# Kernel optimization log

Hardware: AMD Instinct MI355X
Metric: run time of the kernel (lower is better)

## Reference

```python
import jax, jax.numpy as jnp
import numpy as np

F = 128
E = 100000   # num_edges
T = 1000000  # num_triplets


def setup_inputs() -> dict:
    key = jax.random.key(0)
    ks = jax.random.split(key, 20)
    s = 0.05
    return {
        "f": jax.random.normal(ks[0], (E, 2 * F), jnp.float32),
        "M01": jax.random.normal(ks[1], (T, F), jnp.float32),
        "M02": jax.random.normal(ks[2], (T, F), jnp.float32),
        # split_net MLP([2F, 2F, 2F]): Linear -> act -> Linear
        "W1": jax.random.normal(ks[3], (2 * F, 2 * F), jnp.float32) * s,
        "b1": jnp.zeros((2 * F,), jnp.float32),
        "W2": jax.random.normal(ks[4], (2 * F, 2 * F), jnp.float32) * s,
        "b2": jnp.zeros((2 * F,), jnp.float32),
        "Ws01": jax.random.normal(ks[5], (F, F), jnp.float32) * s,
        "bs01": jnp.zeros((F,), jnp.float32),
        "Ws02": jax.random.normal(ks[6], (F, F), jnp.float32) * s,
        "bs02": jnp.zeros((F,), jnp.float32),
        "Ws": jax.random.normal(ks[7], (2 * F, F), jnp.float32) * s,
        "bs": jnp.zeros((F,), jnp.float32),
        "Wout": jax.random.normal(ks[8], (F, F), jnp.float32) * s,
        "bout": jnp.zeros((F,), jnp.float32),
        "num_edges": E,
        "idx_ji": jax.random.randint(ks[9], (T,), 0, E, jnp.int32),
        "idx_ki": jax.random.randint(ks[10], (T,), 0, E, jnp.int32),
    }


def reference(f, M01, M02, W1, b1, W2, b2, Ws01, bs01, Ws02, bs02, Ws, bs,
              Wout, bout, num_edges, idx_ji, idx_ki):
    act = jax.nn.silu
    # f = act(split_net(f)); split_net = Linear -> act -> Linear
    h = act(act(f @ W1 + b1) @ W2 + b2)          # [E, 2F]
    f01, f02 = jnp.split(h, 2, axis=-1)           # [E, F] each
    # triplet interaction: gather -> multiply -> linear -> act
    s01 = act((f01[idx_ki] * M01 * f01[idx_ji]) @ Ws01 + bs01)  # [T, F]
    s02 = act((f02[idx_ki] * M02 * f02[idx_ji]) @ Ws02 + bs02)  # [T, F]
    s = act(jnp.concatenate((s01, s02), axis=-1) @ Ws + bs)     # [T, F]
    # scatter-sum triplets back to edges
    out = jax.ops.segment_sum(s, idx_ji, num_segments=num_edges)  # [E, F]
    return out @ Wout + bout
```

## Files before the change

kernel.cpp:

```cpp
#include <hip/hip_runtime.h>

typedef __attribute__((ext_vector_type(8))) short short8;
typedef __attribute__((ext_vector_type(4))) float f32x4;

__device__ __forceinline__ float silu_f(float x) { return x / (1.0f + __expf(-x)); }

__device__ __forceinline__ unsigned short f2bf(float x) {
  unsigned u = __float_as_uint(x);
  u += 0x7FFFu + ((u >> 16) & 1u);
  return (unsigned short)(u >> 16);
}
__device__ __forceinline__ float bf2f(unsigned short v) {
  return __uint_as_float(((unsigned)v) << 16);
}
__device__ __forceinline__ unsigned cvtpk_bf16(float lo, float hi) {
  unsigned r;
  asm("v_cvt_pk_bf16_f32 %0, %1, %2" : "=v"(r) : "v"(lo), "v"(hi));
  return r;
}

#define LGKM_SB() do { asm volatile("s_waitcnt lgkmcnt(0)" ::: "memory"); \
                       __builtin_amdgcn_sched_barrier(0); } while (0)

__device__ __forceinline__ void prep_one(const float* __restrict__ W,
                                         unsigned short* __restrict__ wh,
                                         unsigned short* __restrict__ wl,
                                         int N, int e)
{
  int k = e / N, n = e % N;
  float w = W[e];
  unsigned short hi = f2bf(w);
  unsigned short lo = f2bf(w - bf2f(hi));
  int kp = k >> 6, kk = k & 63;
  size_t dst = (size_t)kp * N * 64 + (size_t)n * 64 + ((((kk >> 3) ^ (n & 7)) << 3)) + (kk & 7);
  wh[dst] = hi;
  wl[dst] = lo;
}

__global__ void prep_all(const float* __restrict__ W1, unsigned short* w1h, unsigned short* w1l,
                         const float* __restrict__ W2, unsigned short* w2h, unsigned short* w2l,
                         const float* __restrict__ Wo, unsigned short* woh, unsigned short* wol)
{
  int e = blockIdx.x * 256 + threadIdx.x;
  if (e < 256 * 256) {
    prep_one(W1, w1h, w1l, 256, e);
    prep_one(W2, w2h, w2l, 256, e);
  }
  if (e < 128 * 128) prep_one(Wo, woh, wol, 128, e);
}

template<int INBF, int ASPLIT>
__global__ __launch_bounds__(512)
void mlp_gemm(const void* A_, const unsigned short* __restrict__ wh,
              const unsigned short* __restrict__ wl,
              const float* __restrict__ bias, unsigned short* __restrict__ C, int M)
{
  __shared__ unsigned short aTh[64 * 64], aTl[64 * 64];
  __shared__ unsigned short whb[256 * 64], wlb[256 * 64];
  const int tid = threadIdx.x;
  const int lane = tid & 63, wv = tid >> 6;
  const int g = wv & 3, hh = wv >> 2;
  const int l15 = lane & 15, l4 = lane >> 4;
  const int row0 = blockIdx.x * 64;
  const int r = tid >> 3, kseg = (tid & 7) * 8;
  const f32x4 zero4 = {0.f, 0.f, 0.f, 0.f};

  f32x4 acc[8];
#pragma unroll
  for (int nt = 0; nt < 8; nt++) acc[nt] = zero4;

  for (int kp = 0; kp < 4; kp++) {
    {
      const int grow = row0 + r;
      float x[8];
      if (grow < M) {
        if (INBF) {
          short8 v = *(const short8*)((const unsigned short*)A_ + (size_t)grow * 256 + kp * 64 + kseg);
#pragma unroll
          for (int j = 0; j < 8; j++) x[j] = bf2f((unsigned short)v[j]);
        } else {
          const float* ap = (const float*)A_ + (size_t)grow * 256 + kp * 64 + kseg;
          float4 v0 = *(const float4*)ap;
          float4 v1 = *(const float4*)(ap + 4);
          x[0] = v0.x; x[1] = v0.y; x[2] = v0.z; x[3] = v0.w;
          x[4] = v1.x; x[5] = v1.y; x[6] = v1.z; x[7] = v1.w;
        }
      } else {
#pragma unroll
        for (int j = 0; j < 8; j++) x[j] = 0.f;
      }
      union { short8 s; unsigned short us[8]; } H, L;
#pragma unroll
      for (int j = 0; j < 8; j++) {
        H.us[j] = f2bf(x[j]);
        L.us[j] = ASPLIT ? f2bf(x[j] - bf2f(H.us[j])) : (unsigned short)0;
      }
      const int dst = r * 64 + ((((kseg >> 3) ^ (r & 7)) << 3));
      *(short8*)(aTh + dst) = H.s;
      if (ASPLIT) *(short8*)(aTl + dst) = L.s;
    }
    {
      const short8* srcH = (const short8*)(wh + (size_t)kp * 16384);
      const short8* srcL = (const short8*)(wl + (size_t)kp * 16384);
#pragma unroll
      for (int i = 0; i < 4; i++) {
        ((short8*)whb)[tid + 512 * i] = srcH[tid + 512 * i];
        ((short8*)wlb)[tid + 512 * i] = srcL[tid + 512 * i];
      }
    }
    __syncthreads();
#pragma unroll
    for (int ks = 0; ks < 2; ks++) {
      const int arow = 16 * g + l15;
      const int aof = arow * 64 + (((4 * ks + l4) ^ (arow & 7)) << 3);
      short8 ah = *(const short8*)(aTh + aof);
      short8 al = *(const short8*)(aTl + aof);
#pragma unroll
      for (int nt = 0; nt < 8; nt++) {
        const int col = 128 * hh + 16 * nt + l15;
        const int bof = col * 64 + (((4 * ks + l4) ^ (col & 7)) << 3);
        short8 bh = *(const short8*)(whb + bof);
        short8 bl = *(const short8*)(wlb + bof);
        acc[nt] = __builtin_amdgcn_mfma_f32_16x16x32_bf16(ah, bh, acc[nt], 0, 0, 0);
        acc[nt] = __builtin_amdgcn_mfma_f32_16x16x32_bf16(ah, bl, acc[nt], 0, 0, 0);
        if (ASPLIT)
          acc[nt] = __builtin_amdgcn_mfma_f32_16x16x32_bf16(al, bh, acc[nt], 0, 0, 0);
      }
    }
    __syncthreads();
  }
#pragma unroll
  for (int nt = 0; nt < 8; nt++) {
    const int col = 128 * hh + 16 * nt + l15;
    const float bv = bias[col];
#pragma unroll
    for (int i = 0; i < 4; i++) {
      const int row = row0 + 16 * g + 4 * l4 + i;
      if (row < M) C[(size_t)row * 256 + col] = f2bf(silu_f(acc[nt][i] + bv));
    }
  }
}

__global__ __launch_bounds__(512)
void final_gemm(const float* __restrict__ A, const unsigned short* __restrict__ wh,
                const unsigned short* __restrict__ wl,
                const float* __restrict__ bias, float* __restrict__ C, int M)
{
  __shared__ unsigned short aTh[64 * 64], aTl[64 * 64];
  __shared__ unsigned short whb[128 * 64], wlb[128 * 64];
  const int tid = threadIdx.x;
  const int lane = tid & 63, wv = tid >> 6;
  const int g = wv & 3, hh = wv >> 2;
  const int l15 = lane & 15, l4 = lane >> 4;
  const int row0 = blockIdx.x * 64;
  const int r = tid >> 3, kseg = (tid & 7) * 8;
  const f32x4 zero4 = {0.f, 0.f, 0.f, 0.f};

  f32x4 acc[4];
#pragma unroll
  for (int nt = 0; nt < 4; nt++) acc[nt] = zero4;

  for (int kp = 0; kp < 2; kp++) {
    {
      const int grow = row0 + r;
      float x[8];
      if (grow < M) {
        const float* ap = A + (size_t)grow * 128 + kp * 64 + kseg;
        float4 v0 = *(const float4*)ap;
        float4 v1 = *(const float4*)(ap + 4);
        x[0] = v0.x; x[1] = v0.y; x[2] = v0.z; x[3] = v0.w;
        x[4] = v1.x; x[5] = v1.y; x[6] = v1.z; x[7] = v1.w;
      } else {
#pragma unroll
        for (int j = 0; j < 8; j++) x[j] = 0.f;
      }
      union { short8 s; unsigned short us[8]; } H, L;
#pragma unroll
      for (int j = 0; j < 8; j++) {
        H.us[j] = f2bf(x[j]);
        L.us[j] = f2bf(x[j] - bf2f(H.us[j]));
      }
      const int dst = r * 64 + ((((kseg >> 3) ^ (r & 7)) << 3));
      *(short8*)(aTh + dst) = H.s;
      *(short8*)(aTl + dst) = L.s;
    }
    {
      const short8* srcH = (const short8*)(wh + (size_t)kp * 8192);
      const short8* srcL = (const short8*)(wl + (size_t)kp * 8192);
#pragma unroll
      for (int i = 0; i < 2; i++) {
        ((short8*)whb)[tid + 512 * i] = srcH[tid + 512 * i];
        ((short8*)wlb)[tid + 512 * i] = srcL[tid + 512 * i];
      }
    }
    __syncthreads();
#pragma unroll
    for (int ks = 0; ks < 2; ks++) {
      const int arow = 16 * g + l15;
      const int aof = arow * 64 + (((4 * ks + l4) ^ (arow & 7)) << 3);
      short8 ah = *(const short8*)(aTh + aof);
      short8 al = *(const short8*)(aTl + aof);
#pragma unroll
      for (int nt = 0; nt < 4; nt++) {
        const int col = 64 * hh + 16 * nt + l15;
        const int bof = col * 64 + (((4 * ks + l4) ^ (col & 7)) << 3);
        short8 bh = *(const short8*)(whb + bof);
        short8 bl = *(const short8*)(wlb + bof);
        acc[nt] = __builtin_amdgcn_mfma_f32_16x16x32_bf16(ah, bh, acc[nt], 0, 0, 0);
        acc[nt] = __builtin_amdgcn_mfma_f32_16x16x32_bf16(ah, bl, acc[nt], 0, 0, 0);
        acc[nt] = __builtin_amdgcn_mfma_f32_16x16x32_bf16(al, bh, acc[nt], 0, 0, 0);
      }
    }
    __syncthreads();
  }
#pragma unroll
  for (int nt = 0; nt < 4; nt++) {
    const int col = 64 * hh + 16 * nt + l15;
    const float bv = bias[col];
#pragma unroll
    for (int i = 0; i < 4; i++) {
      const int row = row0 + 16 * g + 4 * l4 + i;
      if (row < M) C[(size_t)row * 128 + col] = acc[nt][i] + bv;
    }
  }
}

__global__ void hist_k(const int* __restrict__ ji, int* __restrict__ cnt, int T) {
  int t = blockIdx.x * 256 + threadIdx.x;
  const int stride = gridDim.x * 256;
  for (; t < T; t += stride) atomicAdd(&cnt[ji[t]], 1);
}

__global__ void scan1_k(const int* __restrict__ cnt, int* __restrict__ csum, int E) {
  __shared__ int red[256];
  const int c0 = blockIdx.x * 2048;
  int s = 0;
  for (int i = threadIdx.x; i < 2048; i += 256) {
    int e = c0 + i;
    if (e < E) s += cnt[e];
  }
  red[threadIdx.x] = s;
  __syncthreads();
  for (int o = 128; o > 0; o >>= 1) {
    if (threadIdx.x < o) red[threadIdx.x] += red[threadIdx.x + o];
    __syncthreads();
  }
  if (threadIdx.x == 0) csum[blockIdx.x] = red[0];
}

__global__ void scan2_k(int* __restrict__ csum, int n) {
  if (threadIdx.x == 0 && blockIdx.x == 0) {
    int acc = 0;
    for (int i = 0; i < n; i++) { int v = csum[i]; csum[i] = acc; acc += v; }
  }
}

__global__ void scan3_k(const int* __restrict__ cnt, const int* __restrict__ csum,
                        int* __restrict__ off, int E) {
  __shared__ int ts[256];
  const int c0 = blockIdx.x * 2048;
  const int tid = threadIdx.x;
  int loc[8];
  int s = 0;
#pragma unroll
  for (int k = 0; k < 8; k++) {
    int e = c0 + tid * 8 + k;
    loc[k] = (e < E) ? cnt[e] : 0;
    s += loc[k];
  }
  ts[tid] = s;
  __syncthreads();
  for (int o = 1; o < 256; o <<= 1) {
    int v = (tid >= o) ? ts[tid - o] : 0;
    __syncthreads();
    ts[tid] += v;
    __syncthreads();
  }
  int base = csum[blockIdx.x] + ((tid > 0) ? ts[tid - 1] : 0);
#pragma unroll
  for (int k = 0; k < 8; k++) {
    int e = c0 + tid * 8 + k;
    if (e < E) { off[e] = base; base += loc[k]; }
  }
}

__global__ void scatter_k(const int* __restrict__ ji, int* __restrict__ cursor,
                          int* __restrict__ perm, int T) {
  int t = blockIdx.x * 256 + threadIdx.x;
  const int stride = gridDim.x * 256;
  for (; t < T; t += stride) {
    int e = ji[t];
    int p = atomicAdd(&cursor[e], 1);
    perm[p] = t;
  }
}

__device__ __forceinline__ short8 pack8p(const short8 a, const short8 b,
                                         const float4 m0, const float4 m1)
{
  float p0 = bf2f((unsigned short)a[0]) * m0.x * bf2f((unsigned short)b[0]);
  float p1 = bf2f((unsigned short)a[1]) * m0.y * bf2f((unsigned short)b[1]);
  float p2 = bf2f((unsigned short)a[2]) * m0.z * bf2f((unsigned short)b[2]);
  float p3 = bf2f((unsigned short)a[3]) * m0.w * bf2f((unsigned short)b[3]);
  float p4 = bf2f((unsigned short)a[4]) * m1.x * bf2f((unsigned short)b[4]);
  float p5 = bf2f((unsigned short)a[5]) * m1.y * bf2f((unsigned short)b[5]);
  float p6 = bf2f((unsigned short)a[6]) * m1.z * bf2f((unsigned short)b[6]);
  float p7 = bf2f((unsigned short)a[7]) * m1.w * bf2f((unsigned short)b[7]);
  union { short8 s; unsigned u[4]; } t;
  t.u[0] = cvtpk_bf16(p0, p1);
  t.u[1] = cvtpk_bf16(p2, p3);
  t.u[2] = cvtpk_bf16(p4, p5);
  t.u[3] = cvtpk_bf16(p6, p7);
  return t.s;
}

__global__ __launch_bounds__(512, 2)
void triplet_fused(const unsigned short* __restrict__ h,
                   const float* __restrict__ M01, const float* __restrict__ M02,
                   const float* __restrict__ Ws01, const float* __restrict__ bs01,
                   const float* __restrict__ Ws02, const float* __restrict__ bs02,
                   const float* __restrict__ Ws,   const float* __restrict__ bs,
                   const int* __restrict__ idx_ji, const int* __restrict__ idx_ki,
                   const int* __restrict__ perm,
                   float* __restrict__ out_acc, int T)
{
  __shared__ unsigned short wF01[16384];
  __shared__ unsigned short wF02[16384];
  __shared__ unsigned short wFA[16384];
  __shared__ unsigned short wFB[16384];
  __shared__ unsigned short sbuf[8][2048];

  const int tid = threadIdx.x;
  for (int e = tid; e < 16384; e += 512) {
    const int j = e & 7, ln = (e >> 3) & 63, ks = (e >> 9) & 3, ct = e >> 11;
    const int col = 16 * ct + (ln & 15);
    const int k = 32 * ks + 8 * (ln >> 4) + j;
    const int src = k * 128 + col;
    wF01[e] = f2bf(Ws01[src]);
    wF02[e] = f2bf(Ws02[src]);
    wFA[e]  = f2bf(Ws[src]);
    wFB[e]  = f2bf(Ws[16384 + src]);
  }
  __syncthreads();

  const int lane = tid & 63, wv = tid >> 6;
  const int l15 = lane & 15, l4 = lane >> 4;
  unsigned short* const sb = sbuf[wv];
  const f32x4 zero4 = {0.f, 0.f, 0.f, 0.f};

  float bs01v[8], bs02v[8], bsv[8];
#pragma unroll
  for (int ct = 0; ct < 8; ct++) {
    bs01v[ct] = bs01[16 * ct + l15];
    bs02v[ct] = bs02[16 * ct + l15];
    bsv[ct]   = bs[16 * ct + l15];
  }

  const int nsub = T >> 4;
  const int stride = gridDim.x * 8;
  int sub = blockIdx.x * 8 + wv;

  int pidx = perm[(sub << 4) + l15];
  int ek = idx_ki[pidx], ej = idx_ji[pidx];

  for (; sub < nsub; sub += stride) {
    const unsigned short* fa = h + (size_t)ek * 256 + 8 * l4;
    const unsigned short* fb = h + (size_t)ej * 256 + 8 * l4;
    const float* mm1 = M01 + (size_t)pidx * 128 + 8 * l4;
    const float* mm2 = M02 + (size_t)pidx * 128 + 8 * l4;
    short8 ra1[4], rb1[4], ra2[4], rb2[4];
    float4 rm1[8], rm2[8];
#pragma unroll
    for (int ks = 0; ks < 4; ks++) {
      ra1[ks] = *(const short8*)(fa + 32 * ks);
      rb1[ks] = *(const short8*)(fb + 32 * ks);
      rm1[2 * ks]     = *(const float4*)(mm1 + 32 * ks);
      rm1[2 * ks + 1] = *(const float4*)(mm1 + 32 * ks + 4);
      ra2[ks] = *(const short8*)(fa + 128 + 32 * ks);
      rb2[ks] = *(const short8*)(fb + 128 + 32 * ks);
      rm2[2 * ks]     = *(const float4*)(mm2 + 32 * ks);
      rm2[2 * ks + 1] = *(const float4*)(mm2 + 32 * ks + 4);
    }

    const int subn = sub + stride;
    int sidx = (subn << 4) + l15;
    if (sidx >= T) sidx = T - 1;
    const int pidx_n = perm[sidx];

    f32x4 acc1[8];
#pragma unroll
    for (int ct = 0; ct < 8; ct++) acc1[ct] = zero4;
    __builtin_amdgcn_s_setprio(1);
#pragma unroll
    for (int ks = 0; ks < 4; ks++) {
      const short8 a = pack8p(ra1[ks], rb1[ks], rm1[2 * ks], rm1[2 * ks + 1]);
#pragma unroll
      for (int ct = 0; ct < 8; ct++) {
        const short8 b = *(const short8*)(wF01 + ((ct * 4 + ks) * 64 + lane) * 8);
        acc1[ct] = __builtin_amdgcn_mfma_f32_16x16x32_bf16(a, b, acc1[ct], 0, 0, 0);
      }
    }
    __builtin_amdgcn_s_setprio(0);

#pragma unroll
    for (int ct = 0; ct < 8; ct++) {
      const int chi = 2 * ct + (l15 >> 3);
#pragma unroll
      for (int i = 0; i < 4; i++) {
        const int row = 4 * l4 + i;
        sb[row * 128 + (((chi ^ (row & 7)) << 3)) + (l15 & 7)] =
            f2bf(silu_f(acc1[ct][i] + bs01v[ct]));
      }
    }
    LGKM_SB();
    short8 as1[4];
#pragma unroll
    for (int ks = 0; ks < 4; ks++)
      as1[ks] = *(const short8*)(sb + l15 * 128 + (((4 * ks + l4) ^ (l15 & 7)) << 3));

    f32x4 acc3[8];
#pragma unroll
    for (int ct = 0; ct < 8; ct++) acc3[ct] = zero4;
    __builtin_amdgcn_s_setprio(1);
#pragma unroll
    for (int ks = 0; ks < 4; ks++)
#pragma unroll
      for (int ct = 0; ct < 8; ct++) {
        const short8 b = *(const short8*)(wFA + ((ct * 4 + ks) * 64 + lane) * 8);
        acc3[ct] = __builtin_amdgcn_mfma_f32_16x16x32_bf16(as1[ks], b, acc3[ct], 0, 0, 0);
      }
    __builtin_amdgcn_s_setprio(0);

    const int ekn = idx_ki[pidx_n], ejn = idx_ji[pidx_n];

#pragma unroll
    for (int ct = 0; ct < 8; ct++) acc1[ct] = zero4;
    __builtin_amdgcn_s_setprio(1);
#pragma unroll
    for (int ks = 0; ks < 4; ks++) {
      const short8 a = pack8p(ra2[ks], rb2[ks], rm2[2 * ks], rm2[2 * ks + 1]);
#pragma unroll
      for (int ct = 0; ct < 8; ct++) {
        const short8 b = *(const short8*)(wF02 + ((ct * 4 + ks) * 64 + lane) * 8);
        acc1[ct] = __builtin_amdgcn_mfma_f32_16x16x32_bf16(a, b, acc1[ct], 0, 0, 0);
      }
    }
    __builtin_amdgcn_s_setprio(0);

#pragma unroll
    for (int ct = 0; ct < 8; ct++) {
      const int chi = 2 * ct + (l15 >> 3);
#pragma unroll
      for (int i = 0; i < 4; i++) {
        const int row = 4 * l4 + i;
        sb[row * 128 + (((chi ^ (row & 7)) << 3)) + (l15 & 7)] =
            f2bf(silu_f(acc1[ct][i] + bs02v[ct]));
      }
    }
    LGKM_SB();
    short8 as2[4];
#pragma unroll
    for (int ks = 0; ks < 4; ks++)
      as2[ks] = *(const short8*)(sb + l15 * 128 + (((4 * ks + l4) ^ (l15 & 7)) << 3));

    __builtin_amdgcn_s_setprio(1);
#pragma unroll
    for (int ks = 0; ks < 4; ks++)
#pragma unroll
      for (int ct = 0; ct < 8; ct++) {
        const short8 b = *(const short8*)(wFB + ((ct * 4 + ks) * 64 + lane) * 8);
        acc3[ct] = __builtin_amdgcn_mfma_f32_16x16x32_bf16(as2[ks], b, acc3[ct], 0, 0, 0);
      }
    __builtin_amdgcn_s_setprio(0);

#pragma unroll
    for (int ct = 0; ct < 8; ct++)
#pragma unroll
      for (int i = 0; i < 4; i++)
        acc3[ct][i] = silu_f(acc3[ct][i] + bsv[ct]);

    {
      const int ejp = __shfl_up(ej, 1, 16);
      unsigned bm = (unsigned)(__ballot((l15 > 0) && (ej != ejp)) & 0xFFFFull);
      int fr = 0;
      unsigned rem = bm;
      while (fr < 16) {
        const int nxt = rem ? (__ffs(rem) - 1) : 16;
        rem &= rem - 1;
        const int lr = nxt - 1;
        const int e = __shfl(ej, fr, 16);
        float sv[8];
#pragma unroll
        for (int ct = 0; ct < 8; ct++) {
          float s = 0.f;
#pragma unroll
          for (int i = 0; i < 4; i++) {
            const int rr = 4 * l4 + i;
            s += (rr >= fr && rr <= lr) ? acc3[ct][i] : 0.f;
          }
          s += __shfl_xor(s, 16);
          s += __shfl_xor(s, 32);
          sv[ct] = s;
        }
        float w0, w1;
        if (l4 == 0)      { w0 = sv[0]; w1 = sv[1]; }
        else if (l4 == 1) { w0 = sv[2]; w1 = sv[3]; }
        else if (l4 == 2) { w0 = sv[4]; w1 = sv[5]; }
        else              { w0 = sv[6]; w1 = sv[7]; }
        float* dst = out_acc + (size_t)e * 128 + 32 * l4 + l15;
        if (fr == 0 || lr == 15) {
          atomicAdd(dst, w0);
          atomicAdd(dst + 16, w1);
        } else {
          dst[0] = w0;
          dst[16] = w1;
        }
        fr = nxt;
      }
    }

    pidx = pidx_n; ek = ekn; ej = ejn;
  }
}

extern "C" void kernel_launch(void* const* d_in, const int* in_sizes, int n_in,
                              void* d_out, int out_size, void* d_ws, size_t ws_size,
                              hipStream_t stream)
{
  const float* f    = (const float*)d_in[0];
  const float* M01  = (const float*)d_in[1];
  const float* M02  = (const float*)d_in[2];
  const float* W1   = (const float*)d_in[3];
  const float* b1   = (const float*)d_in[4];
  const float* W2   = (const float*)d_in[5];
  const float* b2   = (const float*)d_in[6];
  const float* Ws01 = (const float*)d_in[7];
  const float* bs01 = (const float*)d_in[8];
  const float* Ws02 = (const float*)d_in[9];
  const float* bs02 = (const float*)d_in[10];
  const float* Ws   = (const float*)d_in[11];
  const float* bs   = (const float*)d_in[12];
  const float* Wout = (const float*)d_in[13];
  const float* bout = (const float*)d_in[14];
  const int* idx_ji = (const int*)d_in[16];
  const int* idx_ki = (const int*)d_in[17];

  const int E = in_sizes[0] / 256;
  const int T = in_sizes[1] / 128;

  char* w = (char*)d_ws;
  unsigned short* hbuf = (unsigned short*)w;
  size_t o = ((size_t)E * 256 * 2 + 255) & ~(size_t)255;
  unsigned short* wt1h = (unsigned short*)(w + o); o += 256 * 256 * 2;
  unsigned short* wt1l = (unsigned short*)(w + o); o += 256 * 256 * 2;
  unsigned short* wt2h = (unsigned short*)(w + o); o += 256 * 256 * 2;
  unsigned short* wt2l = (unsigned short*)(w + o); o += 256 * 256 * 2;
  unsigned short* wtoh = (unsigned short*)(w + o); o += 128 * 128 * 2;
  unsigned short* wtol = (unsigned short*)(w + o); o += 128 * 128 * 2;
  o = (o + 255) & ~(size_t)255;
  int* cnt = (int*)(w + o);  o += ((size_t)E * 4 + 255) & ~(size_t)255;
  int* off = (int*)(w + o);  o += ((size_t)E * 4 + 255) & ~(size_t)255;
  int* csum = (int*)(w + o); o += 4096;
  int* perm = (int*)(w + o);

  float* out_acc = (float*)d_out;
  const int mb = (E + 63) / 64;

  prep_all<<<(256 * 256 + 255) / 256, 256, 0, stream>>>(W1, wt1h, wt1l,
                                                        W2, wt2h, wt2l,
                                                        Wout, wtoh, wtol);

  mlp_gemm<0, 1><<<mb, 512, 0, stream>>>(f, wt1h, wt1l, b1, hbuf, E);
  mlp_gemm<1, 0><<<mb, 512, 0, stream>>>(hbuf, wt2h, wt2l, b2, hbuf, E);

  hipMemsetAsync(cnt, 0, (size_t)E * 4, stream);
  hist_k<<<1024, 256, 0, stream>>>(idx_ji, cnt, T);
  const int nchunks = (E + 2047) / 2048;
  scan1_k<<<nchunks, 256, 0, stream>>>(cnt, csum, E);
  scan2_k<<<1, 64, 0, stream>>>(csum, nchunks);
  scan3_k<<<nchunks, 256, 0, stream>>>(cnt, csum, off, E);
  scatter_k<<<1024, 256, 0, stream>>>(idx_ji, off, perm, T);

  hipMemsetAsync(d_out, 0, (size_t)E * 128 * sizeof(float), stream);

  triplet_fused<<<256, 512, 0, stream>>>(hbuf, M01, M02, Ws01, bs01, Ws02, bs02,
                                         Ws, bs, idx_ji, idx_ki, perm, out_acc, T);

  final_gemm<<<mb, 512, 0, stream>>>(out_acc, wtoh, wtol, bout, out_acc, E);
}
```

Measured before the change: 778.1 us.

## Move triplet weight fragments from LDS to global memory and raise occupancy

Weight conversion into the MFMA fragment layout now runs once in a separate prep kernel writing to workspace, and triplet_fused reads B fragments straight from global (L2/L1) instead of staging 128KB in LDS per block. This frees LDS so launch bounds go to 4 blocks/CU and the grid doubles to 512 blocks, aiming for better latency hiding of the gathers. Biases are folded into the accumulator initialisation and bf16 packing uses the packed convert instruction. The cost is that every MFMA's B operand becomes a global/cache load instead of an LDS read, and tighter register limits may cause spills.

```diff
diff --git a/kernel.cpp b/kernel.cpp
--- a/kernel.cpp
+++ b/kernel.cpp
@@ -47,6 +47,23 @@
     prep_one(W2, w2h, w2l, 256, e);
   }
   if (e < 128 * 128) prep_one(Wo, woh, wol, 128, e);
+}
+
+__global__ void prep_frag(const float* __restrict__ Ws01, const float* __restrict__ Ws02,
+                          const float* __restrict__ Ws,
+                          unsigned short* __restrict__ w01, unsigned short* __restrict__ w02,
+                          unsigned short* __restrict__ wA,  unsigned short* __restrict__ wB)
+{
+  int e = blockIdx.x * 256 + threadIdx.x;
+  if (e >= 16384) return;
+  const int j = e & 7, ln = (e >> 3) & 63, ks = (e >> 9) & 3, ct = e >> 11;
+  const int col = 16 * ct + (ln & 15);
+  const int k = 32 * ks + 8 * (ln >> 4) + j;
+  const int src = k * 128 + col;
+  w01[e] = f2bf(Ws01[src]);
+  w02[e] = f2bf(Ws02[src]);
+  wA[e]  = f2bf(Ws[src]);
+  wB[e]  = f2bf(Ws[16384 + src]);
 }
 
 template<int INBF, int ASPLIT>
@@ -314,39 +331,25 @@
   return t.s;
 }
 
-__global__ __launch_bounds__(512, 2)
+__global__ __launch_bounds__(512, 4)
 void triplet_fused(const unsigned short* __restrict__ h,
                    const float* __restrict__ M01, const float* __restrict__ M02,
-                   const float* __restrict__ Ws01, const float* __restrict__ bs01,
-                   const float* __restrict__ Ws02, const float* __restrict__ bs02,
-                   const float* __restrict__ Ws,   const float* __restrict__ bs,
+                   const unsigned short* __restrict__ wF01,
+                   const unsigned short* __restrict__ wF02,
+                   const unsigned short* __restrict__ wFA,
+                   const unsigned short* __restrict__ wFB,
+                   const float* __restrict__ bs01, const float* __restrict__ bs02,
+                   const float* __restrict__ bs,
                    const int* __restrict__ idx_ji, const int* __restrict__ idx_ki,
                    const int* __restrict__ perm,
                    float* __restrict__ out_acc, int T)
 {
-  __shared__ unsigned short wF01[16384];
-  __shared__ unsigned short wF02[16384];
-  __shared__ unsigned short wFA[16384];
-  __shared__ unsigned short wFB[16384];
   __shared__ unsigned short sbuf[8][2048];
 
   const int tid = threadIdx.x;
-  for (int e = tid; e < 16384; e += 512) {
-    const int j = e & 7, ln = (e >> 3) & 63, ks = (e >> 9) & 3, ct = e >> 11;
-    const int col = 16 * ct + (ln & 15);
-    const int k = 32 * ks + 8 * (ln >> 4) + j;
-    const int src = k * 128 + col;
-    wF01[e] = f2bf(Ws01[src]);
-    wF02[e] = f2bf(Ws02[src]);
-    wFA[e]  = f2bf(Ws[src]);
-    wFB[e]  = f2bf(Ws[16384 + src]);
-  }
-  __syncthreads();
-
   const int lane = tid & 63, wv = tid >> 6;
   const int l15 = lane & 15, l4 = lane >> 4;
   unsigned short* const sb = sbuf[wv];
-  const f32x4 zero4 = {0.f, 0.f, 0.f, 0.f};
 
   float bs01v[8], bs02v[8], bsv[8];
 #pragma unroll
@@ -359,6 +362,7 @@
   const int nsub = T >> 4;
   const int stride = gridDim.x * 8;
   int sub = blockIdx.x * 8 + wv;
+  if (sub >= nsub) return;
 
   int pidx = perm[(sub << 4) + l15];
   int ek = idx_ki[pidx], ej = idx_ji[pidx];
@@ -389,7 +393,10 @@
 
     f32x4 acc1[8];
 #pragma unroll
-    for (int ct = 0; ct < 8; ct++) acc1[ct] = zero4;
+    for (int ct = 0; ct < 8; ct++) {
+      const float b = bs01v[ct];
+      acc1[ct] = (f32x4){b, b, b, b};
+    }
     __builtin_amdgcn_s_setprio(1);
 #pragma unroll
     for (int ks = 0; ks < 4; ks++) {
@@ -405,12 +412,17 @@
 #pragma unroll
     for (int ct = 0; ct < 8; ct++) {
       const int chi = 2 * ct + (l15 >> 3);
-#pragma unroll
-      for (int i = 0; i < 4; i++) {
-        const int row = 4 * l4 + i;
-        sb[row * 128 + (((chi ^ (row & 7)) << 3)) + (l15 & 7)] =
-            f2bf(silu_f(acc1[ct][i] + bs01v[ct]));
-      }
+      const float s0 = silu_f(acc1[ct][0]);
+      const float s1 = silu_f(acc1[ct][1]);
+      const float s2 = silu_f(acc1[ct][2]);
+      const float s3 = silu_f(acc1[ct][3]);
+      const unsigned u01 = cvtpk_bf16(s0, s1);
+      const unsigned u23 = cvtpk_bf16(s2, s3);
+      const int r0 = 4 * l4;
+      sb[(r0 + 0) * 128 + (((chi ^ ((r0 + 0) & 7)) << 3)) + (l15 & 7)] = (unsigned short)u01;
+      sb[(r0 + 1) * 128 + (((chi ^ ((r0 + 1) & 7)) << 3)) + (l15 & 7)] = (unsigned short)(u01 >> 16);
+      sb[(r0 + 2) * 128 + (((chi ^ ((r0 + 2) & 7)) << 3)) + (l15 & 7)] = (unsigned short)u23;
+      sb[(r0 + 3) * 128 + (((chi ^ ((r0 + 3) & 7)) << 3)) + (l15 & 7)] = (unsigned short)(u23 >> 16);
     }
     LGKM_SB();
     short8 as1[4];
@@ -420,7 +432,10 @@
 
     f32x4 acc3[8];
 #pragma unroll
-    for (int ct = 0; ct < 8; ct++) acc3[ct] = zero4;
+    for (int ct = 0; ct < 8; ct++) {
+      const float b = bsv[ct];
+      acc3[ct] = (f32x4){b, b, b, b};
+    }
     __builtin_amdgcn_s_setprio(1);
 #pragma unroll
     for (int ks = 0; ks < 4; ks++)
@@ -434,7 +449,10 @@
     const int ekn = idx_ki[pidx_n], ejn = idx_ji[pidx_n];
 
 #pragma unroll
-    for (int ct = 0; ct < 8; ct++) acc1[ct] = zero4;
+    for (int ct = 0; ct < 8; ct++) {
+      const float b = bs02v[ct];
+      acc1[ct] = (f32x4){b, b, b, b};
+    }
     __builtin_amdgcn_s_setprio(1);
 #pragma unroll
     for (int ks = 0; ks < 4; ks++) {
@@ -450,12 +468,17 @@
 #pragma unroll
     for (int ct = 0; ct < 8; ct++) {
       const int chi = 2 * ct + (l15 >> 3);
-#pragma unroll
-      for (int i = 0; i < 4; i++) {
-        const int row = 4 * l4 + i;
-        sb[row * 128 + (((chi ^ (row & 7)) << 3)) + (l15 & 7)] =
-            f2bf(silu_f(acc1[ct][i] + bs02v[ct]));
-      }
+      const float s0 = silu_f(acc1[ct][0]);
+      const float s1 = silu_f(acc1[ct][1]);
+      const float s2 = silu_f(acc1[ct][2]);
+      const float s3 = silu_f(acc1[ct][3]);
+      const unsigned u01 = cvtpk_bf16(s0, s1);
+      const unsigned u23 = cvtpk_bf16(s2, s3);
+      const int r0 = 4 * l4;
+      sb[(r0 + 0) * 128 + (((chi ^ ((r0 + 0) & 7)) << 3)) + (l15 & 7)] = (unsigned short)u01;
+      sb[(r0 + 1) * 128 + (((chi ^ ((r0 + 1) & 7)) << 3)) + (l15 & 7)] = (unsigned short)(u01 >> 16);
+      sb[(r0 + 2) * 128 + (((chi ^ ((r0 + 2) & 7)) << 3)) + (l15 & 7)] = (unsigned short)u23;
+      sb[(r0 + 3) * 128 + (((chi ^ ((r0 + 3) & 7)) << 3)) + (l15 & 7)] = (unsigned short)(u23 >> 16);
     }
     LGKM_SB();
     short8 as2[4];
@@ -477,7 +500,7 @@
     for (int ct = 0; ct < 8; ct++)
 #pragma unroll
       for (int i = 0; i < 4; i++)
-        acc3[ct][i] = silu_f(acc3[ct][i] + bsv[ct]);
+        acc3[ct][i] = silu_f(acc3[ct][i]);
 
     {
       const int ejp = __shfl_up(ej, 1, 16);
@@ -557,6 +580,10 @@
   unsigned short* wt2l = (unsigned short*)(w + o); o += 256 * 256 * 2;
   unsigned short* wtoh = (unsigned short*)(w + o); o += 128 * 128 * 2;
   unsigned short* wtol = (unsigned short*)(w + o); o += 128 * 128 * 2;
+  unsigned short* wf01 = (unsigned short*)(w + o); o += 16384 * 2;
+  unsigned short* wf02 = (unsigned short*)(w + o); o += 16384 * 2;
+  unsigned short* wfA  = (unsigned short*)(w + o); o += 16384 * 2;
+  unsigned short* wfB  = (unsigned short*)(w + o); o += 16384 * 2;
   o = (o + 255) & ~(size_t)255;
   int* cnt = (int*)(w + o);  o += ((size_t)E * 4 + 255) & ~(size_t)255;
   int* off = (int*)(w + o);  o += ((size_t)E * 4 + 255) & ~(size_t)255;
@@ -569,6 +596,7 @@
   prep_all<<<(256 * 256 + 255) / 256, 256, 0, stream>>>(W1, wt1h, wt1l,
                                                         W2, wt2h, wt2l,
                                                         Wout, wtoh, wtol);
+  prep_frag<<<64, 256, 0, stream>>>(Ws01, Ws02, Ws, wf01, wf02, wfA, wfB);
 
   mlp_gemm<0, 1><<<mb, 512, 0, stream>>>(f, wt1h, wt1l, b1, hbuf, E);
   mlp_gemm<1, 0><<<mb, 512, 0, stream>>>(hbuf, wt2h, wt2l, b2, hbuf, E);
@@ -583,8 +611,9 @@
 
   hipMemsetAsync(d_out, 0, (size_t)E * 128 * sizeof(float), stream);
 
-  triplet_fused<<<256, 512, 0, stream>>>(hbuf, M01, M02, Ws01, bs01, Ws02, bs02,
-                                         Ws, bs, idx_ji, idx_ki, perm, out_acc, T);
+  triplet_fused<<<512, 512, 0, stream>>>(hbuf, M01, M02, wf01, wf02, wfA, wfB,
+                                         bs01, bs02, bs, idx_ji, idx_ki, perm,
+                                         out_acc, T);
 
   final_gemm<<<mb, 512, 0, stream>>>(out_acc, wtoh, wtol, bout, out_acc, E);
 }
```

Result: slower. 2.822 ms (+262.7%).
